# Performance work log

Measured on AMD Instinct MI355X. Metric: run time of the kernel, lower is better.

The kernel has to match this reference:

```python
import jax
import jax.numpy as jnp
import numpy as np
from jax import lax

B, L, H, M = 32768, 128, 256, 16


def setup_inputs() -> dict:
    key = jax.random.key(0)
    ks = jax.random.split(key, 7)
    s_ih = 1.0 / np.sqrt(H)  # PyTorch GRUCell init scale (uniform bound); use scaled normal
    return {
        "x": jax.random.randint(ks[0], (B, L), 0, M, dtype=jnp.int32),
        "W_ih": jax.random.normal(ks[1], (3 * H, 1), dtype=jnp.float32) * s_ih,
        "W_hh": jax.random.normal(ks[2], (3 * H, H), dtype=jnp.float32) * s_ih,
        "b_ih": jax.random.normal(ks[3], (3 * H,), dtype=jnp.float32) * s_ih,
        "b_hh": jax.random.normal(ks[4], (3 * H,), dtype=jnp.float32) * s_ih,
        "W_fc": jax.random.normal(ks[5], (M, H), dtype=jnp.float32) * s_ih,
        "b_fc": jax.random.normal(ks[6], (M,), dtype=jnp.float32) * s_ih,
    }


def reference(x, W_ih, W_hh, b_ih, b_hh, W_fc, b_fc):
    # (zeros at i=0) as a scalar feature; output log_softmax gathered at x[:, i].
    xf = x.astype(jnp.float32)
    x_in = jnp.concatenate([jnp.zeros((x.shape[0], 1), jnp.float32), xf[:, :-1]], axis=1)  # [B, L]

    def step(h, inp):
        x_t, tgt = inp  # x_t: [B] float, tgt: [B] int
        gi = x_t[:, None] * W_ih.T + b_ih            # [B, 3H] (input dim is 1)
        gh = h @ W_hh.T + b_hh                       # [B, 3H]
        ir, iz, i_n = jnp.split(gi, 3, axis=1)
        hr, hz, h_n = jnp.split(gh, 3, axis=1)
        r = jax.nn.sigmoid(ir + hr)
        z = jax.nn.sigmoid(iz + hz)
        n = jnp.tanh(i_n + r * h_n)
        h_new = (1.0 - z) * n + z * h                # [B, H]
        logp = jax.nn.log_softmax(h_new @ W_fc.T + b_fc, axis=1)  # [B, M]
        lp = jnp.take_along_axis(logp, tgt[:, None], axis=1)[:, 0]  # [B]
        return h_new, lp

    h0 = jnp.zeros((x.shape[0], W_hh.shape[1]), jnp.float32)
    _, lps = lax.scan(step, h0, (x_in.T, x.T))  # lps: [L, B]
    return lps.sum(axis=0)  # [B] log_probsum
```

## Files before the change

kernel.cpp:

```cpp
#include <hip/hip_runtime.h>

typedef __attribute__((ext_vector_type(8))) short s16x8;
typedef __attribute__((ext_vector_type(4))) float f32x4;

#define BATCH 32768
#define LSEQ 128
#define NJT 16
#define NFRAG 28
#define WFRAG_SHORTS (NJT * NFRAG * 512)
#define WFC_SHORTS 4096
#define XT_OFF_BYTES ((WFRAG_SHORTS + WFC_SHORTS) * 2)
#define WS_NEED_XT (XT_OFF_BYTES + BATCH * LSEQ * 4)

#define HBUF_SHORTS (128 * 256)
#define LDS_BYTES (2 * HBUF_SHORTS * 2 + WFC_SHORTS * 2)

#define L2E 1.4426950408889634f
#define LN2 0.6931471805599453f

__device__ __forceinline__ unsigned short f2b(float f) {
  unsigned u = __float_as_uint(f);
  u += 0x7FFFu + ((u >> 16) & 1u);
  return (unsigned short)(u >> 16);
}

__device__ __forceinline__ float exp2n(float x) { float r; asm("v_exp_f32 %0, -%1" : "=v"(r) : "v"(x)); return r; }
__device__ __forceinline__ float exp2p(float x) { float r; asm("v_exp_f32 %0, %1" : "=v"(r) : "v"(x)); return r; }
__device__ __forceinline__ float rcp_(float x)  { float r; asm("v_rcp_f32 %0, %1" : "=v"(r) : "v"(x)); return r; }
__device__ __forceinline__ float log2_(float x) { float r; asm("v_log_f32 %0, %1" : "=v"(r) : "v"(x)); return r; }
__device__ __forceinline__ unsigned cvtpk(float lo, float hi) {
  unsigned r; asm("v_cvt_pk_bf16_f32 %0, %1, %2" : "=v"(r) : "v"(lo), "v"(hi)); return r;
}

__global__ void gru_prep(const float* __restrict__ Wih, const float* __restrict__ Whh,
                         const float* __restrict__ bih, const float* __restrict__ bhh,
                         const float* __restrict__ Wfc,
                         unsigned short* __restrict__ wfrag,
                         unsigned short* __restrict__ wfc16) {
  int t = blockIdx.x * 256 + threadIdx.x;
  if (t < WFRAG_SHORTS) {
    int e = t & 7, lane = (t >> 3) & 63, fl = t >> 9;
    int f = fl % NFRAG, jt = fl / NFRAG;
    int m = lane & 15, gl = lane >> 4;
    float val = 0.f;
    if (f < 27) {
      int g = f / 9, ks = f % 9;
      int row = g * 256 + jt * 16 + m;
      int k = ks * 32 + gl * 8 + e;
      float sc = (g == 2) ? 2.f * L2E : L2E;
      if (k < 256) val = Whh[row * 256 + k] * sc;
      else if (k == 256) val = (g == 2) ? 0.f : Wih[row] * sc;
      else if (k == 257) val = ((g == 2) ? bhh[row] : (bih[row] + bhh[row])) * sc;
    }
    wfrag[t] = f2b(val);
  } else if (t < WFRAG_SHORTS + WFC_SHORTS) {
    int t2 = t - WFRAG_SHORTS;
    wfc16[t2] = f2b(Wfc[t2] * L2E);
  }
}

__global__ void x_transpose(const int* __restrict__ x, int* __restrict__ xT) {
  __shared__ int tile[32][33];
  int l0 = blockIdx.x * 32, b0 = blockIdx.y * 32;
  for (int r = threadIdx.y; r < 32; r += 8)
    tile[r][threadIdx.x] = x[(b0 + r) * LSEQ + l0 + threadIdx.x];
  __syncthreads();
  for (int r = threadIdx.y; r < 32; r += 8)
    xT[(l0 + r) * BATCH + b0 + threadIdx.x] = tile[threadIdx.x][r];
}

__device__ __forceinline__ int haddr(int lrow, int col_s) {
  return lrow * 256 + ((col_s + ((lrow & 15) << 3)) & 255);
}

template <int XT>
__global__ __attribute__((amdgpu_waves_per_eu(2, 2))) __launch_bounds__(512)
void gru_main(const int* __restrict__ x, const int* __restrict__ xTr,
              const unsigned short* __restrict__ wfrag,
              const unsigned short* __restrict__ wfc16,
              const float* __restrict__ Wih, const float* __restrict__ bih,
              const float* __restrict__ bfc, float* __restrict__ out) {
  extern __shared__ unsigned short smem_us[];
  unsigned short* h0 = smem_us;
  unsigned short* h1 = smem_us + HBUF_SHORTS;
  unsigned short* wl = smem_us + 2 * HBUF_SHORTS;

  const int tid = threadIdx.x;
  const int lane = tid & 63;
  const int wv = tid >> 6;
  const int q = lane >> 4;
  const int b = lane & 15;
  const int bbase = blockIdx.x * 128;

  {
    unsigned int* p = (unsigned int*)h0;
#pragma unroll
    for (int r = 0; r < 32; ++r) p[tid + r * 512] = 0u;
  }
  for (int t = tid; t < WFC_SHORTS; t += 512) {
    int m = t >> 8, col = t & 255;
    wl[haddr(m, col)] = wfc16[t];
  }

  float win0[4], bin0[4], win1[4], bin1[4];
#pragma unroll
  for (int r = 0; r < 4; ++r) {
    int j0 = 512 + wv * 16 + q * 4 + r;
    int j1 = 512 + (wv + 8) * 16 + q * 4 + r;
    win0[r] = Wih[j0] * (2.f * L2E);  bin0[r] = bih[j0] * (2.f * L2E);
    win1[r] = Wih[j1] * (2.f * L2E);  bin1[r] = bih[j1] * (2.f * L2E);
  }
  float bfc4[4];
#pragma unroll
  for (int r = 0; r < 4; ++r) bfc4[r] = bfc[q * 4 + r] * L2E;

  float lp = 0.f;
  __syncthreads();

#pragma unroll 1
  for (int i = 0; i < LSEQ; ++i) {
    const unsigned short* rd = (i & 1) ? h1 : h0;
    unsigned short* wr = (i & 1) ? h0 : h1;

    unsigned long wfu = (unsigned long)wfrag;
    asm volatile("" : "+s"(wfu));
    const unsigned short* wf = (const unsigned short*)wfu;

    float xin8[8];
    unsigned xlo[8];
#pragma unroll
    for (int bt = 0; bt < 8; ++bt) {
      float xv;
      if (XT) xv = (i > 0) ? (float)xTr[(i - 1) * BATCH + bbase + bt * 16 + b] : 0.f;
      else    xv = (i > 0) ? (float)x[(bbase + bt * 16 + b) * LSEQ + i - 1] : 0.f;
      xin8[bt] = xv;
      xlo[bt] = (q == 0) ? ((__float_as_uint(xv) >> 16) | 0x3F800000u) : 0u;
    }

#pragma unroll 1
    for (int ph = 0; ph < 2; ++ph) {
      const int jt = wv + 8 * ph;
      const unsigned short* fb = wf + (jt * NFRAG * 64 + lane) * 8;

      f32x4 aR[8], aZ[8], aH[8];
      const f32x4 Z = {0.f, 0.f, 0.f, 0.f};

      s16x8 ar = *(const s16x8*)(fb + 8 * 512);
      s16x8 az = *(const s16x8*)(fb + 17 * 512);
      s16x8 ah = *(const s16x8*)(fb + 26 * 512);
      s16x8 cr = *(const s16x8*)(fb);
      s16x8 cz = *(const s16x8*)(fb + 9 * 512);
      s16x8 ch = *(const s16x8*)(fb + 18 * 512);

#pragma unroll
      for (int bt = 0; bt < 8; ++bt) {
        union { unsigned u[4]; s16x8 v; } xf;
        xf.u[0] = xlo[bt]; xf.u[1] = 0u; xf.u[2] = 0u; xf.u[3] = 0u;
        aR[bt] = __builtin_amdgcn_mfma_f32_16x16x32_bf16(ar, xf.v, Z, 0, 0, 0);
        aZ[bt] = __builtin_amdgcn_mfma_f32_16x16x32_bf16(az, xf.v, Z, 0, 0, 0);
        aH[bt] = __builtin_amdgcn_mfma_f32_16x16x32_bf16(ah, xf.v, Z, 0, 0, 0);
      }

      auto burst = [&](s16x8 A0, s16x8 A1, s16x8 A2, int ks) {
#pragma unroll
        for (int bt = 0; bt < 8; ++bt) {
          const s16x8 hb = *(const s16x8*)&rd[haddr(bt * 16 + b, 32 * ks + 8 * q)];
          aR[bt] = __builtin_amdgcn_mfma_f32_16x16x32_bf16(A0, hb, aR[bt], 0, 0, 0);
          aZ[bt] = __builtin_amdgcn_mfma_f32_16x16x32_bf16(A1, hb, aZ[bt], 0, 0, 0);
          aH[bt] = __builtin_amdgcn_mfma_f32_16x16x32_bf16(A2, hb, aH[bt], 0, 0, 0);
        }
      };

#pragma unroll 1
      for (int ks = 0; ks < 7; ++ks) {
        s16x8 nr = *(const s16x8*)(fb + (ks + 1) * 512);
        s16x8 nz = *(const s16x8*)(fb + (ks + 10) * 512);
        s16x8 nh = *(const s16x8*)(fb + (ks + 19) * 512);
        burst(cr, cz, ch, ks);
        cr = nr; cz = nz; ch = nh;
      }
      burst(cr, cz, ch, 7);

      const float wcA = ph ? win1[0] : win0[0], wcB = ph ? win1[1] : win0[1];
      const float wcC = ph ? win1[2] : win0[2], wcD = ph ? win1[3] : win0[3];
      const float bcA = ph ? bin1[0] : bin0[0], bcB = ph ? bin1[1] : bin0[1];
      const float bcC = ph ? bin1[2] : bin0[2], bcD = ph ? bin1[3] : bin0[3];
#pragma unroll
      for (int bt = 0; bt < 8; ++bt) {
        const int lrow = bt * 16 + b;
        const uint2 hp = *(const uint2*)&rd[haddr(lrow, 16 * jt + 4 * q)];
        const float xv = xin8[bt];
        const float inr[4] = {fmaf(xv, wcA, bcA), fmaf(xv, wcB, bcB),
                              fmaf(xv, wcC, bcC), fmaf(xv, wcD, bcD)};
        const float hpv[4] = {
            __uint_as_float(hp.x << 16), __uint_as_float(hp.x & 0xFFFF0000u),
            __uint_as_float(hp.y << 16), __uint_as_float(hp.y & 0xFFFF0000u)};
        float hv[4];
#pragma unroll
        for (int r = 0; r < 4; ++r) {
          float rr = rcp_(1.f + exp2n(aR[bt][r]));
          float zz = rcp_(1.f + exp2n(aZ[bt][r]));
          float y  = fmaf(rr, aH[bt][r], inr[r]);
          float u  = rcp_(1.f + exp2p(y));
          float nn = fmaf(-2.f, u, 1.f);
          hv[r] = fmaf(zz, hpv[r] - nn, nn);
        }
        *(uint2*)&wr[haddr(lrow, 16 * jt + 4 * q)] =
            make_uint2(cvtpk(hv[0], hv[1]), cvtpk(hv[2], hv[3]));
      }
    }

    __syncthreads();

    {
      const int lrow = wv * 16 + b;
      const int grow = bbase + lrow;
      f32x4 fa = {bfc4[0], bfc4[1], bfc4[2], bfc4[3]};
#pragma unroll
      for (int ks = 0; ks < 8; ++ks) {
        s16x8 wfcf = *(const s16x8*)&wl[haddr(b, 32 * ks + 8 * q)];
        s16x8 hb = *(const s16x8*)&wr[haddr(lrow, 32 * ks + 8 * q)];
        fa = __builtin_amdgcn_mfma_f32_16x16x32_bf16(wfcf, hb, fa, 0, 0, 0);
      }
      int tgt = XT ? xTr[i * BATCH + grow] : x[grow * LSEQ + i];
      float l0 = fa[0], l1 = fa[1], l2 = fa[2], l3 = fa[3];
      float mx = fmaxf(fmaxf(l0, l1), fmaxf(l2, l3));
      mx = fmaxf(mx, __shfl_xor(mx, 16));
      mx = fmaxf(mx, __shfl_xor(mx, 32));
      float se = exp2p(l0 - mx) + exp2p(l1 - mx) + exp2p(l2 - mx) + exp2p(l3 - mx);
      se += __shfl_xor(se, 16);
      se += __shfl_xor(se, 32);
      float v01 = (tgt & 1) ? l1 : l0;
      float v23 = (tgt & 1) ? l3 : l2;
      float vs = (tgt & 2) ? v23 : v01;
      float contrib = (q == (tgt >> 2)) ? vs : 0.f;
      contrib += __shfl_xor(contrib, 16);
      contrib += __shfl_xor(contrib, 32);
      lp += contrib - mx - log2_(se);
    }
  }

  if (q == 0) out[bbase + wv * 16 + b] = lp * LN2;
}

extern "C" void kernel_launch(void* const* d_in, const int* in_sizes, int n_in,
                              void* d_out, int out_size, void* d_ws, size_t ws_size,
                              hipStream_t stream) {
  (void)in_sizes; (void)n_in; (void)out_size;
  const int*   x   = (const int*)d_in[0];
  const float* Wih = (const float*)d_in[1];
  const float* Whh = (const float*)d_in[2];
  const float* bih = (const float*)d_in[3];
  const float* bhh = (const float*)d_in[4];
  const float* Wfc = (const float*)d_in[5];
  const float* bfc = (const float*)d_in[6];
  float* out = (float*)d_out;

  unsigned short* wfrag = (unsigned short*)d_ws;
  unsigned short* wfc16 = wfrag + WFRAG_SHORTS;
  int* xT = (int*)((char*)d_ws + XT_OFF_BYTES);

  gru_prep<<<dim3(912), dim3(256), 0, stream>>>(Wih, Whh, bih, bhh, Wfc, wfrag, wfc16);

  if (ws_size >= (size_t)WS_NEED_XT) {
    x_transpose<<<dim3(LSEQ / 32, BATCH / 32), dim3(32, 8), 0, stream>>>(x, xT);
    hipFuncSetAttribute((const void*)gru_main<1>,
                        hipFuncAttributeMaxDynamicSharedMemorySize, LDS_BYTES);
    gru_main<1><<<dim3(256), dim3(512), LDS_BYTES, stream>>>(x, xT, wfrag, wfc16,
                                                             Wih, bih, bfc, out);
  } else {
    hipFuncSetAttribute((const void*)gru_main<0>,
                        hipFuncAttributeMaxDynamicSharedMemorySize, LDS_BYTES);
    gru_main<0><<<dim3(256), dim3(512), LDS_BYTES, stream>>>(x, x, wfrag, wfc16,
                                                             Wih, bih, bfc, out);
  }
}
```

Measured before the change: 1.847 ms.

## Switch GRU recurrence to 32x32x16 MFMA tiles with padded LDS rows

Replaces the 16x16x32 MFMA tiling of the hidden-state GEMM with 32x32x16 MFMAs. Each wave now owns a 32-wide hidden slice across all gates and processes pairs of 32-row batch groups, with the input-gate term folded in as an extra MFMA. The XOR-swizzled LDS layout is replaced by rows padded to 264 elements. The FC weights are read from global memory instead of LDS, and the log2e scaling moves from the prepacked weights into the epilogue. The aim is fewer MFMA issues and more reuse per weight fragment, at the cost of extra epilogue multiplies and possible register pressure from the larger accumulators.

```diff
diff --git a/kernel.cpp b/kernel.cpp
--- a/kernel.cpp
+++ b/kernel.cpp
@@ -2,21 +2,23 @@
 
 typedef __attribute__((ext_vector_type(8))) short s16x8;
 typedef __attribute__((ext_vector_type(4))) float f32x4;
+typedef __attribute__((ext_vector_type(16))) float f32x16;
 
 #define BATCH 32768
 #define LSEQ 128
-#define NJT 16
-#define NFRAG 28
-#define WFRAG_SHORTS (NJT * NFRAG * 512)
+#define W32_SHORTS (8 * 4 * 17 * 512)
 #define WFC_SHORTS 4096
-#define XT_OFF_BYTES ((WFRAG_SHORTS + WFC_SHORTS) * 2)
+#define XT_OFF_BYTES ((W32_SHORTS + WFC_SHORTS) * 2)
 #define WS_NEED_XT (XT_OFF_BYTES + BATCH * LSEQ * 4)
 
-#define HBUF_SHORTS (128 * 256)
-#define LDS_BYTES (2 * HBUF_SHORTS * 2 + WFC_SHORTS * 2)
+#define HROW 264
+#define HBUF_S (128 * HROW)
+#define LDS_BYTES (2 * HBUF_S * 2)
 
 #define L2E 1.4426950408889634f
 #define LN2 0.6931471805599453f
+
+#define MFMA32(A, B, C) __builtin_amdgcn_mfma_f32_32x32x16_bf16(A, B, C, 0, 0, 0)
 
 __device__ __forceinline__ unsigned short f2b(float f) {
   unsigned u = __float_as_uint(f);
@@ -38,24 +40,26 @@
                          unsigned short* __restrict__ wfrag,
                          unsigned short* __restrict__ wfc16) {
   int t = blockIdx.x * 256 + threadIdx.x;
-  if (t < WFRAG_SHORTS) {
-    int e = t & 7, lane = (t >> 3) & 63, fl = t >> 9;
-    int f = fl % NFRAG, jt = fl / NFRAG;
-    int m = lane & 15, gl = lane >> 4;
+  if (t < W32_SHORTS) {
+    int e = t & 7, lane = (t >> 3) & 63, frag = t >> 9;
+    int ks = frag % 17, g = (frag / 17) & 3, tr = frag / 68;
+    int l31 = lane & 31, hh = lane >> 5;
+    int k = (ks < 16) ? ks * 16 + hh * 8 + e : 256 + hh * 8 + e;
     float val = 0.f;
-    if (f < 27) {
-      int g = f / 9, ks = f % 9;
-      int row = g * 256 + jt * 16 + m;
-      int k = ks * 32 + gl * 8 + e;
-      float sc = (g == 2) ? 2.f * L2E : L2E;
-      if (k < 256) val = Whh[row * 256 + k] * sc;
-      else if (k == 256) val = (g == 2) ? 0.f : Wih[row] * sc;
-      else if (k == 257) val = ((g == 2) ? bhh[row] : (bih[row] + bhh[row])) * sc;
+    if (g < 3) {
+      int j = g * 256 + tr * 32 + l31;
+      if (k < 256) val = Whh[j * 256 + k];
+      else if (k == 256) val = (g < 2) ? Wih[j] : 0.f;
+      else if (k == 257) val = (g < 2) ? (bih[j] + bhh[j]) : bhh[j];
+    } else if (ks == 16) {
+      int j = 512 + tr * 32 + l31;
+      if (k == 256) val = Wih[j];
+      else if (k == 257) val = bih[j];
     }
     wfrag[t] = f2b(val);
-  } else if (t < WFRAG_SHORTS + WFC_SHORTS) {
-    int t2 = t - WFRAG_SHORTS;
-    wfc16[t2] = f2b(Wfc[t2] * L2E);
+  } else if (t < W32_SHORTS + WFC_SHORTS) {
+    int t2 = t - W32_SHORTS;
+    wfc16[t2] = f2b(Wfc[t2]);
   }
 }
 
@@ -69,145 +73,151 @@
     xT[(l0 + r) * BATCH + b0 + threadIdx.x] = tile[threadIdx.x][r];
 }
 
-__device__ __forceinline__ int haddr(int lrow, int col_s) {
-  return lrow * 256 + ((col_s + ((lrow & 15) << 3)) & 255);
-}
-
 template <int XT>
 __global__ __attribute__((amdgpu_waves_per_eu(2, 2))) __launch_bounds__(512)
 void gru_main(const int* __restrict__ x, const int* __restrict__ xTr,
               const unsigned short* __restrict__ wfrag,
               const unsigned short* __restrict__ wfc16,
-              const float* __restrict__ Wih, const float* __restrict__ bih,
               const float* __restrict__ bfc, float* __restrict__ out) {
-  extern __shared__ unsigned short smem_us[];
-  unsigned short* h0 = smem_us;
-  unsigned short* h1 = smem_us + HBUF_SHORTS;
-  unsigned short* wl = smem_us + 2 * HBUF_SHORTS;
+  extern __shared__ unsigned short sm[];
 
   const int tid = threadIdx.x;
   const int lane = tid & 63;
   const int wv = tid >> 6;
+  const int tr = wv;
+  const int l31 = lane & 31;
+  const int hh = lane >> 5;
   const int q = lane >> 4;
   const int b = lane & 15;
   const int bbase = blockIdx.x * 128;
 
   {
-    unsigned int* p = (unsigned int*)h0;
-#pragma unroll
-    for (int r = 0; r < 32; ++r) p[tid + r * 512] = 0u;
-  }
-  for (int t = tid; t < WFC_SHORTS; t += 512) {
-    int m = t >> 8, col = t & 255;
-    wl[haddr(m, col)] = wfc16[t];
-  }
-
-  float win0[4], bin0[4], win1[4], bin1[4];
-#pragma unroll
-  for (int r = 0; r < 4; ++r) {
-    int j0 = 512 + wv * 16 + q * 4 + r;
-    int j1 = 512 + (wv + 8) * 16 + q * 4 + r;
-    win0[r] = Wih[j0] * (2.f * L2E);  bin0[r] = bih[j0] * (2.f * L2E);
-    win1[r] = Wih[j1] * (2.f * L2E);  bin1[r] = bih[j1] * (2.f * L2E);
-  }
+    unsigned int* p = (unsigned int*)sm;
+    for (int r = tid; r < HBUF_S / 2; r += 512) p[r] = 0u;
+  }
+
   float bfc4[4];
 #pragma unroll
-  for (int r = 0; r < 4; ++r) bfc4[r] = bfc[q * 4 + r] * L2E;
+  for (int r = 0; r < 4; ++r) bfc4[r] = bfc[q * 4 + r];
+
+  const int offR = ((tr * 4 + 0) * 17) * 512 + lane * 8;
+  const int offZ = ((tr * 4 + 1) * 17) * 512 + lane * 8;
+  const int offH = ((tr * 4 + 2) * 17) * 512 + lane * 8;
+  const int offI = ((tr * 4 + 3) * 17) * 512 + lane * 8;
+  const int offFC = b * 256 + q * 8;
+
+  const f32x16 z16 = {0, 0, 0, 0, 0, 0, 0, 0, 0, 0, 0, 0, 0, 0, 0, 0};
 
   float lp = 0.f;
   __syncthreads();
 
 #pragma unroll 1
   for (int i = 0; i < LSEQ; ++i) {
-    const unsigned short* rd = (i & 1) ? h1 : h0;
-    unsigned short* wr = (i & 1) ? h0 : h1;
+    const unsigned short* rdb = sm + (i & 1) * HBUF_S;
+    unsigned short* wrb = sm + ((i & 1) ^ 1) * HBUF_S;
 
     unsigned long wfu = (unsigned long)wfrag;
     asm volatile("" : "+s"(wfu));
-    const unsigned short* wf = (const unsigned short*)wfu;
-
-    float xin8[8];
-    unsigned xlo[8];
-#pragma unroll
-    for (int bt = 0; bt < 8; ++bt) {
-      float xv;
-      if (XT) xv = (i > 0) ? (float)xTr[(i - 1) * BATCH + bbase + bt * 16 + b] : 0.f;
-      else    xv = (i > 0) ? (float)x[(bbase + bt * 16 + b) * LSEQ + i - 1] : 0.f;
-      xin8[bt] = xv;
-      xlo[bt] = (q == 0) ? ((__float_as_uint(xv) >> 16) | 0x3F800000u) : 0u;
-    }
-
-#pragma unroll 1
-    for (int ph = 0; ph < 2; ++ph) {
-      const int jt = wv + 8 * ph;
-      const unsigned short* fb = wf + (jt * NFRAG * 64 + lane) * 8;
-
-      f32x4 aR[8], aZ[8], aH[8];
-      const f32x4 Z = {0.f, 0.f, 0.f, 0.f};
-
-      s16x8 ar = *(const s16x8*)(fb + 8 * 512);
-      s16x8 az = *(const s16x8*)(fb + 17 * 512);
-      s16x8 ah = *(const s16x8*)(fb + 26 * 512);
-      s16x8 cr = *(const s16x8*)(fb);
-      s16x8 cz = *(const s16x8*)(fb + 9 * 512);
-      s16x8 ch = *(const s16x8*)(fb + 18 * 512);
-
-#pragma unroll
-      for (int bt = 0; bt < 8; ++bt) {
-        union { unsigned u[4]; s16x8 v; } xf;
-        xf.u[0] = xlo[bt]; xf.u[1] = 0u; xf.u[2] = 0u; xf.u[3] = 0u;
-        aR[bt] = __builtin_amdgcn_mfma_f32_16x16x32_bf16(ar, xf.v, Z, 0, 0, 0);
-        aZ[bt] = __builtin_amdgcn_mfma_f32_16x16x32_bf16(az, xf.v, Z, 0, 0, 0);
-        aH[bt] = __builtin_amdgcn_mfma_f32_16x16x32_bf16(ah, xf.v, Z, 0, 0, 0);
+    const unsigned short* wfp = (const unsigned short*)wfu;
+    const unsigned short* fR = wfp + offR;
+    const unsigned short* fZ = wfp + offZ;
+    const unsigned short* fH = wfp + offH;
+    const unsigned short* fI = wfp + offI;
+    unsigned long wcu = (unsigned long)wfc16;
+    asm volatile("" : "+s"(wcu));
+    const unsigned short* fFC = (const unsigned short*)wcu + offFC;
+
+#pragma unroll
+    for (int p = 0; p < 2; ++p) {
+      const int b0 = 2 * p, b1 = 2 * p + 1;
+
+      float xv0, xv1;
+      if (XT) {
+        xv0 = (i > 0) ? (float)xTr[(i - 1) * BATCH + bbase + b0 * 32 + l31] : 0.f;
+        xv1 = (i > 0) ? (float)xTr[(i - 1) * BATCH + bbase + b1 * 32 + l31] : 0.f;
+      } else {
+        xv0 = (i > 0) ? (float)x[(bbase + b0 * 32 + l31) * LSEQ + i - 1] : 0.f;
+        xv1 = (i > 0) ? (float)x[(bbase + b1 * 32 + l31) * LSEQ + i - 1] : 0.f;
       }
-
-      auto burst = [&](s16x8 A0, s16x8 A1, s16x8 A2, int ks) {
-#pragma unroll
-        for (int bt = 0; bt < 8; ++bt) {
-          const s16x8 hb = *(const s16x8*)&rd[haddr(bt * 16 + b, 32 * ks + 8 * q)];
-          aR[bt] = __builtin_amdgcn_mfma_f32_16x16x32_bf16(A0, hb, aR[bt], 0, 0, 0);
-          aZ[bt] = __builtin_amdgcn_mfma_f32_16x16x32_bf16(A1, hb, aZ[bt], 0, 0, 0);
-          aH[bt] = __builtin_amdgcn_mfma_f32_16x16x32_bf16(A2, hb, aH[bt], 0, 0, 0);
+      union { unsigned u[4]; s16x8 v; } xf0, xf1;
+      xf0.u[0] = (hh == 0) ? ((__float_as_uint(xv0) >> 16) | 0x3F800000u) : 0u;
+      xf0.u[1] = xf0.u[2] = xf0.u[3] = 0u;
+      xf1.u[0] = (hh == 0) ? ((__float_as_uint(xv1) >> 16) | 0x3F800000u) : 0u;
+      xf1.u[1] = xf1.u[2] = xf1.u[3] = 0u;
+
+      s16x8 gR = *(const s16x8*)(fR + 16 * 512);
+      s16x8 gZ = *(const s16x8*)(fZ + 16 * 512);
+      s16x8 gH = *(const s16x8*)(fH + 16 * 512);
+      s16x8 gI = *(const s16x8*)(fI + 16 * 512);
+      f32x16 R0 = MFMA32(gR, xf0.v, z16), R1 = MFMA32(gR, xf1.v, z16);
+      f32x16 Z0 = MFMA32(gZ, xf0.v, z16), Z1 = MFMA32(gZ, xf1.v, z16);
+      f32x16 H0 = MFMA32(gH, xf0.v, z16), H1 = MFMA32(gH, xf1.v, z16);
+      f32x16 I0 = MFMA32(gI, xf0.v, z16), I1 = MFMA32(gI, xf1.v, z16);
+
+      s16x8 c0r = *(const s16x8*)(fR + 0 * 512);
+      s16x8 c0z = *(const s16x8*)(fZ + 0 * 512);
+      s16x8 c0h = *(const s16x8*)(fH + 0 * 512);
+      s16x8 c1r = *(const s16x8*)(fR + 1 * 512);
+      s16x8 c1z = *(const s16x8*)(fZ + 1 * 512);
+      s16x8 c1h = *(const s16x8*)(fH + 1 * 512);
+
+      const unsigned short* r0b = rdb + (b0 * 32 + l31) * HROW;
+      const unsigned short* r1b = rdb + (b1 * 32 + l31) * HROW;
+
+#pragma unroll
+      for (int it = 0; it < 8; ++it) {
+        s16x8 n0r, n0z, n0h, n1r, n1z, n1h;
+        if (it < 7) {
+          n0r = *(const s16x8*)(fR + (2 * it + 2) * 512);
+          n0z = *(const s16x8*)(fZ + (2 * it + 2) * 512);
+          n0h = *(const s16x8*)(fH + (2 * it + 2) * 512);
+          n1r = *(const s16x8*)(fR + (2 * it + 3) * 512);
+          n1z = *(const s16x8*)(fZ + (2 * it + 3) * 512);
+          n1h = *(const s16x8*)(fH + (2 * it + 3) * 512);
+        }
+        {
+          const s16x8 hA = *(const s16x8*)&r0b[16 * (2 * it) + 8 * hh];
+          const s16x8 hB = *(const s16x8*)&r1b[16 * (2 * it) + 8 * hh];
+          R0 = MFMA32(c0r, hA, R0); Z0 = MFMA32(c0z, hA, Z0); H0 = MFMA32(c0h, hA, H0);
+          R1 = MFMA32(c0r, hB, R1); Z1 = MFMA32(c0z, hB, Z1); H1 = MFMA32(c0h, hB, H1);
+        }
+        {
+          const s16x8 hA = *(const s16x8*)&r0b[16 * (2 * it + 1) + 8 * hh];
+          const s16x8 hB = *(const s16x8*)&r1b[16 * (2 * it + 1) + 8 * hh];
+          R0 = MFMA32(c1r, hA, R0); Z0 = MFMA32(c1z, hA, Z0); H0 = MFMA32(c1h, hA, H0);
+          R1 = MFMA32(c1r, hB, R1); Z1 = MFMA32(c1z, hB, Z1); H1 = MFMA32(c1h, hB, H1);
+        }
+        if (it < 7) { c0r = n0r; c0z = n0z; c0h = n0h; c1r = n1r; c1z = n1z; c1h = n1h; }
+      }
+
+      auto epilogue = [&](int bg, const f32x16& R, const f32x16& Zg,
+                          const f32x16& Hg, const f32x16& Ig) {
+        const int hrow = bg * 32 + l31;
+        const unsigned short* hpb = rdb + hrow * HROW;
+        unsigned short* hwb = wrb + hrow * HROW;
+#pragma unroll
+        for (int rq = 0; rq < 4; ++rq) {
+          const int col = tr * 32 + 4 * hh + 8 * rq;
+          const uint2 hp = *(const uint2*)&hpb[col];
+          const float hpv[4] = {
+              __uint_as_float(hp.x << 16), __uint_as_float(hp.x & 0xFFFF0000u),
+              __uint_as_float(hp.y << 16), __uint_as_float(hp.y & 0xFFFF0000u)};
+          float hv[4];
+#pragma unroll
+          for (int e2 = 0; e2 < 4; ++e2) {
+            const int idx = rq * 4 + e2;
+            float rr = rcp_(1.f + exp2n(L2E * R[idx]));
+            float zz = rcp_(1.f + exp2n(L2E * Zg[idx]));
+            float y  = fmaf(rr, Hg[idx], Ig[idx]);
+            float u  = rcp_(1.f + exp2p((2.f * L2E) * y));
+            float nn = fmaf(-2.f, u, 1.f);
+            hv[e2] = fmaf(zz, hpv[e2] - nn, nn);
+          }
+          *(uint2*)&hwb[col] = make_uint2(cvtpk(hv[0], hv[1]), cvtpk(hv[2], hv[3]));
         }
       };
-
-#pragma unroll 1
-      for (int ks = 0; ks < 7; ++ks) {
-        s16x8 nr = *(const s16x8*)(fb + (ks + 1) * 512);
-        s16x8 nz = *(const s16x8*)(fb + (ks + 10) * 512);
-        s16x8 nh = *(const s16x8*)(fb + (ks + 19) * 512);
-        burst(cr, cz, ch, ks);
-        cr = nr; cz = nz; ch = nh;
-      }
-      burst(cr, cz, ch, 7);
-
-      const float wcA = ph ? win1[0] : win0[0], wcB = ph ? win1[1] : win0[1];
-      const float wcC = ph ? win1[2] : win0[2], wcD = ph ? win1[3] : win0[3];
-      const float bcA = ph ? bin1[0] : bin0[0], bcB = ph ? bin1[1] : bin0[1];
-      const float bcC = ph ? bin1[2] : bin0[2], bcD = ph ? bin1[3] : bin0[3];
-#pragma unroll
-      for (int bt = 0; bt < 8; ++bt) {
-        const int lrow = bt * 16 + b;
-        const uint2 hp = *(const uint2*)&rd[haddr(lrow, 16 * jt + 4 * q)];
-        const float xv = xin8[bt];
-        const float inr[4] = {fmaf(xv, wcA, bcA), fmaf(xv, wcB, bcB),
-                              fmaf(xv, wcC, bcC), fmaf(xv, wcD, bcD)};
-        const float hpv[4] = {
-            __uint_as_float(hp.x << 16), __uint_as_float(hp.x & 0xFFFF0000u),
-            __uint_as_float(hp.y << 16), __uint_as_float(hp.y & 0xFFFF0000u)};
-        float hv[4];
-#pragma unroll
-        for (int r = 0; r < 4; ++r) {
-          float rr = rcp_(1.f + exp2n(aR[bt][r]));
-          float zz = rcp_(1.f + exp2n(aZ[bt][r]));
-          float y  = fmaf(rr, aH[bt][r], inr[r]);
-          float u  = rcp_(1.f + exp2p(y));
-          float nn = fmaf(-2.f, u, 1.f);
-          hv[r] = fmaf(zz, hpv[r] - nn, nn);
-        }
-        *(uint2*)&wr[haddr(lrow, 16 * jt + 4 * q)] =
-            make_uint2(cvtpk(hv[0], hv[1]), cvtpk(hv[2], hv[3]));
-      }
+      epilogue(b0, R0, Z0, H0, I0);
+      epilogue(b1, R1, Z1, H1, I1);
     }
 
     __syncthreads();
@@ -216,18 +226,20 @@
       const int lrow = wv * 16 + b;
       const int grow = bbase + lrow;
       f32x4 fa = {bfc4[0], bfc4[1], bfc4[2], bfc4[3]};
+      const unsigned short* hbb = wrb + lrow * HROW;
 #pragma unroll
       for (int ks = 0; ks < 8; ++ks) {
-        s16x8 wfcf = *(const s16x8*)&wl[haddr(b, 32 * ks + 8 * q)];
-        s16x8 hb = *(const s16x8*)&wr[haddr(lrow, 32 * ks + 8 * q)];
-        fa = __builtin_amdgcn_mfma_f32_16x16x32_bf16(wfcf, hb, fa, 0, 0, 0);
+        s16x8 wf = *(const s16x8*)(fFC + 32 * ks);
+        s16x8 hb = *(const s16x8*)&hbb[32 * ks + 8 * q];
+        fa = __builtin_amdgcn_mfma_f32_16x16x32_bf16(wf, hb, fa, 0, 0, 0);
       }
       int tgt = XT ? xTr[i * BATCH + grow] : x[grow * LSEQ + i];
       float l0 = fa[0], l1 = fa[1], l2 = fa[2], l3 = fa[3];
       float mx = fmaxf(fmaxf(l0, l1), fmaxf(l2, l3));
       mx = fmaxf(mx, __shfl_xor(mx, 16));
       mx = fmaxf(mx, __shfl_xor(mx, 32));
-      float se = exp2p(l0 - mx) + exp2p(l1 - mx) + exp2p(l2 - mx) + exp2p(l3 - mx);
+      float se = exp2p(L2E * (l0 - mx)) + exp2p(L2E * (l1 - mx)) +
+                 exp2p(L2E * (l2 - mx)) + exp2p(L2E * (l3 - mx));
       se += __shfl_xor(se, 16);
       se += __shfl_xor(se, 32);
       float v01 = (tgt & 1) ? l1 : l0;
@@ -236,11 +248,11 @@
       float contrib = (q == (tgt >> 2)) ? vs : 0.f;
       contrib += __shfl_xor(contrib, 16);
       contrib += __shfl_xor(contrib, 32);
-      lp += contrib - mx - log2_(se);
+      lp += contrib - mx - LN2 * log2_(se);
     }
   }
 
-  if (q == 0) out[bbase + wv * 16 + b] = lp * LN2;
+  if (q == 0) out[bbase + wv * 16 + b] = lp;
 }
 
 extern "C" void kernel_launch(void* const* d_in, const int* in_sizes, int n_in,
@@ -257,21 +269,20 @@
   float* out = (float*)d_out;
 
   unsigned short* wfrag = (unsigned short*)d_ws;
-  unsigned short* wfc16 = wfrag + WFRAG_SHORTS;
+  unsigned short* wfc16 = wfrag + W32_SHORTS;
   int* xT = (int*)((char*)d_ws + XT_OFF_BYTES);
 
-  gru_prep<<<dim3(912), dim3(256), 0, stream>>>(Wih, Whh, bih, bhh, Wfc, wfrag, wfc16);
+  gru_prep<<<dim3((W32_SHORTS + WFC_SHORTS) / 256), dim3(256), 0, stream>>>(
+      Wih, Whh, bih, bhh, Wfc, wfrag, wfc16);
 
   if (ws_size >= (size_t)WS_NEED_XT) {
     x_transpose<<<dim3(LSEQ / 32, BATCH / 32), dim3(32, 8), 0, stream>>>(x, xT);
     hipFuncSetAttribute((const void*)gru_main<1>,
                         hipFuncAttributeMaxDynamicSharedMemorySize, LDS_BYTES);
-    gru_main<1><<<dim3(256), dim3(512), LDS_BYTES, stream>>>(x, xT, wfrag, wfc16,
-                                                             Wih, bih, bfc, out);
+    gru_main<1><<<dim3(256), dim3(512), LDS_BYTES, stream>>>(x, xT, wfrag, wfc16, bfc, out);
   } else {
     hipFuncSetAttribute((const void*)gru_main<0>,
                         hipFuncAttributeMaxDynamicSharedMemorySize, LDS_BYTES);
-    gru_main<0><<<dim3(256), dim3(512), LDS_BYTES, stream>>>(x, x, wfrag, wfc16,
-                                                             Wih, bih, bfc, out);
-  }
-}
+    gru_main<0><<<dim3(256), dim3(512), LDS_BYTES, stream>>>(x, x, wfrag, wfc16, bfc, out);
+  }
+}
```

After: 2.042 ms. 10.6% more time.

## Pad LDS hidden-state rows, read W_fc from global, fully unroll K loop

Applied to the files above, without the earlier changes.

Replaces the XOR-swizzled hidden-state layout with rows padded to 264 shorts to avoid LDS bank conflicts using simpler address arithmetic. The W_fc copy in LDS is dropped and W_fc fragments are read straight from global/L2. The K-loop over weight fragments is fully unrolled, with all 24 weight fragments loaded up front instead of double-buffered. The log2e scaling moves from the prepped weights into the activation math, which costs extra multiplies per element and may change bf16 rounding of the weights. The extra fragment registers raise register pressure.

```diff
diff --git a/kernel.cpp b/kernel.cpp
--- a/kernel.cpp
+++ b/kernel.cpp
@@ -12,11 +12,14 @@
 #define XT_OFF_BYTES ((WFRAG_SHORTS + WFC_SHORTS) * 2)
 #define WS_NEED_XT (XT_OFF_BYTES + BATCH * LSEQ * 4)
 
-#define HBUF_SHORTS (128 * 256)
-#define LDS_BYTES (2 * HBUF_SHORTS * 2 + WFC_SHORTS * 2)
+#define HROW 264
+#define HBUF_S (128 * HROW)
+#define LDS_BYTES (2 * HBUF_S * 2)
 
 #define L2E 1.4426950408889634f
 #define LN2 0.6931471805599453f
+
+#define MFMA16(A, B, C) __builtin_amdgcn_mfma_f32_16x16x32_bf16(A, B, C, 0, 0, 0)
 
 __device__ __forceinline__ unsigned short f2b(float f) {
   unsigned u = __float_as_uint(f);
@@ -47,15 +50,14 @@
       int g = f / 9, ks = f % 9;
       int row = g * 256 + jt * 16 + m;
       int k = ks * 32 + gl * 8 + e;
-      float sc = (g == 2) ? 2.f * L2E : L2E;
-      if (k < 256) val = Whh[row * 256 + k] * sc;
-      else if (k == 256) val = (g == 2) ? 0.f : Wih[row] * sc;
-      else if (k == 257) val = ((g == 2) ? bhh[row] : (bih[row] + bhh[row])) * sc;
+      if (k < 256) val = Whh[row * 256 + k];
+      else if (k == 256) val = (g == 2) ? 0.f : Wih[row];
+      else if (k == 257) val = (g == 2) ? bhh[row] : (bih[row] + bhh[row]);
     }
     wfrag[t] = f2b(val);
   } else if (t < WFRAG_SHORTS + WFC_SHORTS) {
     int t2 = t - WFRAG_SHORTS;
-    wfc16[t2] = f2b(Wfc[t2] * L2E);
+    wfc16[t2] = f2b(Wfc[t2]);
   }
 }
 
@@ -69,10 +71,6 @@
     xT[(l0 + r) * BATCH + b0 + threadIdx.x] = tile[threadIdx.x][r];
 }
 
-__device__ __forceinline__ int haddr(int lrow, int col_s) {
-  return lrow * 256 + ((col_s + ((lrow & 15) << 3)) & 255);
-}
-
 template <int XT>
 __global__ __attribute__((amdgpu_waves_per_eu(2, 2))) __launch_bounds__(512)
 void gru_main(const int* __restrict__ x, const int* __restrict__ xTr,
@@ -80,10 +78,9 @@
               const unsigned short* __restrict__ wfc16,
               const float* __restrict__ Wih, const float* __restrict__ bih,
               const float* __restrict__ bfc, float* __restrict__ out) {
-  extern __shared__ unsigned short smem_us[];
-  unsigned short* h0 = smem_us;
-  unsigned short* h1 = smem_us + HBUF_SHORTS;
-  unsigned short* wl = smem_us + 2 * HBUF_SHORTS;
+  extern __shared__ unsigned short sm[];
+  unsigned short* h0 = sm;
+  unsigned short* h1 = sm + HBUF_S;
 
   const int tid = threadIdx.x;
   const int lane = tid & 63;
@@ -95,11 +92,7 @@
   {
     unsigned int* p = (unsigned int*)h0;
 #pragma unroll
-    for (int r = 0; r < 32; ++r) p[tid + r * 512] = 0u;
-  }
-  for (int t = tid; t < WFC_SHORTS; t += 512) {
-    int m = t >> 8, col = t & 255;
-    wl[haddr(m, col)] = wfc16[t];
+    for (int r = 0; r < 33; ++r) p[tid + r * 512] = 0u;
   }
 
   float win0[4], bin0[4], win1[4], bin1[4];
@@ -107,12 +100,14 @@
   for (int r = 0; r < 4; ++r) {
     int j0 = 512 + wv * 16 + q * 4 + r;
     int j1 = 512 + (wv + 8) * 16 + q * 4 + r;
-    win0[r] = Wih[j0] * (2.f * L2E);  bin0[r] = bih[j0] * (2.f * L2E);
-    win1[r] = Wih[j1] * (2.f * L2E);  bin1[r] = bih[j1] * (2.f * L2E);
+    win0[r] = Wih[j0];  bin0[r] = bih[j0];
+    win1[r] = Wih[j1];  bin1[r] = bih[j1];
   }
   float bfc4[4];
 #pragma unroll
-  for (int r = 0; r < 4; ++r) bfc4[r] = bfc[q * 4 + r] * L2E;
+  for (int r = 0; r < 4; ++r) bfc4[r] = bfc[q * 4 + r];
+
+  const int rbase = b * HROW + 8 * q;
 
   float lp = 0.f;
   __syncthreads();
@@ -125,61 +120,67 @@
     unsigned long wfu = (unsigned long)wfrag;
     asm volatile("" : "+s"(wfu));
     const unsigned short* wf = (const unsigned short*)wfu;
+    unsigned long wcu = (unsigned long)wfc16;
+    asm volatile("" : "+s"(wcu));
+    const unsigned short* wc = (const unsigned short*)wcu;
 
     float xin8[8];
-    unsigned xlo[8];
 #pragma unroll
     for (int bt = 0; bt < 8; ++bt) {
-      float xv;
-      if (XT) xv = (i > 0) ? (float)xTr[(i - 1) * BATCH + bbase + bt * 16 + b] : 0.f;
-      else    xv = (i > 0) ? (float)x[(bbase + bt * 16 + b) * LSEQ + i - 1] : 0.f;
-      xin8[bt] = xv;
-      xlo[bt] = (q == 0) ? ((__float_as_uint(xv) >> 16) | 0x3F800000u) : 0u;
+      if (XT) xin8[bt] = (i > 0) ? (float)xTr[(i - 1) * BATCH + bbase + bt * 16 + b] : 0.f;
+      else    xin8[bt] = (i > 0) ? (float)x[(bbase + bt * 16 + b) * LSEQ + i - 1] : 0.f;
     }
 
 #pragma unroll 1
     for (int ph = 0; ph < 2; ++ph) {
       const int jt = wv + 8 * ph;
       const unsigned short* fb = wf + (jt * NFRAG * 64 + lane) * 8;
-
-      f32x4 aR[8], aZ[8], aH[8];
-      const f32x4 Z = {0.f, 0.f, 0.f, 0.f};
+      const unsigned short* rdT = rd + rbase;
 
       s16x8 ar = *(const s16x8*)(fb + 8 * 512);
       s16x8 az = *(const s16x8*)(fb + 17 * 512);
       s16x8 ah = *(const s16x8*)(fb + 26 * 512);
-      s16x8 cr = *(const s16x8*)(fb);
-      s16x8 cz = *(const s16x8*)(fb + 9 * 512);
-      s16x8 ch = *(const s16x8*)(fb + 18 * 512);
-
+      s16x8 c0r = *(const s16x8*)(fb + 0 * 512), c0z = *(const s16x8*)(fb + 9 * 512),  c0h = *(const s16x8*)(fb + 18 * 512);
+      s16x8 c1r = *(const s16x8*)(fb + 1 * 512), c1z = *(const s16x8*)(fb + 10 * 512), c1h = *(const s16x8*)(fb + 19 * 512);
+      s16x8 c2r = *(const s16x8*)(fb + 2 * 512), c2z = *(const s16x8*)(fb + 11 * 512), c2h = *(const s16x8*)(fb + 20 * 512);
+      s16x8 c3r = *(const s16x8*)(fb + 3 * 512), c3z = *(const s16x8*)(fb + 12 * 512), c3h = *(const s16x8*)(fb + 21 * 512);
+
+      f32x4 aR[8], aZ[8], aH[8];
+      const f32x4 Z4 = {0.f, 0.f, 0.f, 0.f};
 #pragma unroll
       for (int bt = 0; bt < 8; ++bt) {
         union { unsigned u[4]; s16x8 v; } xf;
-        xf.u[0] = xlo[bt]; xf.u[1] = 0u; xf.u[2] = 0u; xf.u[3] = 0u;
-        aR[bt] = __builtin_amdgcn_mfma_f32_16x16x32_bf16(ar, xf.v, Z, 0, 0, 0);
-        aZ[bt] = __builtin_amdgcn_mfma_f32_16x16x32_bf16(az, xf.v, Z, 0, 0, 0);
-        aH[bt] = __builtin_amdgcn_mfma_f32_16x16x32_bf16(ah, xf.v, Z, 0, 0, 0);
+        xf.u[0] = (q == 0) ? ((__float_as_uint(xin8[bt]) >> 16) | 0x3F800000u) : 0u;
+        xf.u[1] = xf.u[2] = xf.u[3] = 0u;
+        aR[bt] = MFMA16(ar, xf.v, Z4);
+        aZ[bt] = MFMA16(az, xf.v, Z4);
+        aH[bt] = MFMA16(ah, xf.v, Z4);
       }
 
-      auto burst = [&](s16x8 A0, s16x8 A1, s16x8 A2, int ks) {
-#pragma unroll
-        for (int bt = 0; bt < 8; ++bt) {
-          const s16x8 hb = *(const s16x8*)&rd[haddr(bt * 16 + b, 32 * ks + 8 * q)];
-          aR[bt] = __builtin_amdgcn_mfma_f32_16x16x32_bf16(A0, hb, aR[bt], 0, 0, 0);
-          aZ[bt] = __builtin_amdgcn_mfma_f32_16x16x32_bf16(A1, hb, aZ[bt], 0, 0, 0);
-          aH[bt] = __builtin_amdgcn_mfma_f32_16x16x32_bf16(A2, hb, aH[bt], 0, 0, 0);
-        }
-      };
-
-#pragma unroll 1
-      for (int ks = 0; ks < 7; ++ks) {
-        s16x8 nr = *(const s16x8*)(fb + (ks + 1) * 512);
-        s16x8 nz = *(const s16x8*)(fb + (ks + 10) * 512);
-        s16x8 nh = *(const s16x8*)(fb + (ks + 19) * 512);
-        burst(cr, cz, ch, ks);
-        cr = nr; cz = nz; ch = nh;
-      }
-      burst(cr, cz, ch, 7);
+      s16x8 n0r = *(const s16x8*)(fb + 4 * 512), n0z = *(const s16x8*)(fb + 13 * 512), n0h = *(const s16x8*)(fb + 22 * 512);
+      s16x8 n1r = *(const s16x8*)(fb + 5 * 512), n1z = *(const s16x8*)(fb + 14 * 512), n1h = *(const s16x8*)(fb + 23 * 512);
+      s16x8 n2r = *(const s16x8*)(fb + 6 * 512), n2z = *(const s16x8*)(fb + 15 * 512), n2h = *(const s16x8*)(fb + 24 * 512);
+      s16x8 n3r = *(const s16x8*)(fb + 7 * 512), n3z = *(const s16x8*)(fb + 16 * 512), n3h = *(const s16x8*)(fb + 25 * 512);
+
+#define BURST(CR, CZ, CH, KS)                                                   \
+  {                                                                             \
+    _Pragma("unroll")                                                           \
+    for (int bt = 0; bt < 8; ++bt) {                                            \
+      const s16x8 hb = *(const s16x8*)&rdT[bt * 16 * HROW + 32 * (KS)];         \
+      aR[bt] = MFMA16(CR, hb, aR[bt]);                                          \
+      aZ[bt] = MFMA16(CZ, hb, aZ[bt]);                                          \
+      aH[bt] = MFMA16(CH, hb, aH[bt]);                                          \
+    }                                                                           \
+  }
+      BURST(c0r, c0z, c0h, 0)
+      BURST(c1r, c1z, c1h, 1)
+      BURST(c2r, c2z, c2h, 2)
+      BURST(c3r, c3z, c3h, 3)
+      BURST(n0r, n0z, n0h, 4)
+      BURST(n1r, n1z, n1h, 5)
+      BURST(n2r, n2z, n2h, 6)
+      BURST(n3r, n3z, n3h, 7)
+#undef BURST
 
       const float wcA = ph ? win1[0] : win0[0], wcB = ph ? win1[1] : win0[1];
       const float wcC = ph ? win1[2] : win0[2], wcD = ph ? win1[3] : win0[3];
@@ -188,7 +189,7 @@
 #pragma unroll
       for (int bt = 0; bt < 8; ++bt) {
         const int lrow = bt * 16 + b;
-        const uint2 hp = *(const uint2*)&rd[haddr(lrow, 16 * jt + 4 * q)];
+        const uint2 hp = *(const uint2*)&rd[lrow * HROW + 16 * jt + 4 * q];
         const float xv = xin8[bt];
         const float inr[4] = {fmaf(xv, wcA, bcA), fmaf(xv, wcB, bcB),
                               fmaf(xv, wcC, bcC), fmaf(xv, wcD, bcD)};
@@ -198,14 +199,14 @@
         float hv[4];
 #pragma unroll
         for (int r = 0; r < 4; ++r) {
-          float rr = rcp_(1.f + exp2n(aR[bt][r]));
-          float zz = rcp_(1.f + exp2n(aZ[bt][r]));
+          float rr = rcp_(1.f + exp2n(L2E * aR[bt][r]));
+          float zz = rcp_(1.f + exp2n(L2E * aZ[bt][r]));
           float y  = fmaf(rr, aH[bt][r], inr[r]);
-          float u  = rcp_(1.f + exp2p(y));
+          float u  = rcp_(1.f + exp2p((2.f * L2E) * y));
           float nn = fmaf(-2.f, u, 1.f);
           hv[r] = fmaf(zz, hpv[r] - nn, nn);
         }
-        *(uint2*)&wr[haddr(lrow, 16 * jt + 4 * q)] =
+        *(uint2*)&wr[lrow * HROW + 16 * jt + 4 * q] =
             make_uint2(cvtpk(hv[0], hv[1]), cvtpk(hv[2], hv[3]));
       }
     }
@@ -216,18 +217,21 @@
       const int lrow = wv * 16 + b;
       const int grow = bbase + lrow;
       f32x4 fa = {bfc4[0], bfc4[1], bfc4[2], bfc4[3]};
+      const unsigned short* hbb = wr + lrow * HROW + 8 * q;
+      const unsigned short* wcb = wc + b * 256 + q * 8;
 #pragma unroll
       for (int ks = 0; ks < 8; ++ks) {
-        s16x8 wfcf = *(const s16x8*)&wl[haddr(b, 32 * ks + 8 * q)];
-        s16x8 hb = *(const s16x8*)&wr[haddr(lrow, 32 * ks + 8 * q)];
-        fa = __builtin_amdgcn_mfma_f32_16x16x32_bf16(wfcf, hb, fa, 0, 0, 0);
+        s16x8 wfcf = *(const s16x8*)(wcb + 32 * ks);
+        s16x8 hb = *(const s16x8*)(hbb + 32 * ks);
+        fa = MFMA16(wfcf, hb, fa);
       }
       int tgt = XT ? xTr[i * BATCH + grow] : x[grow * LSEQ + i];
       float l0 = fa[0], l1 = fa[1], l2 = fa[2], l3 = fa[3];
       float mx = fmaxf(fmaxf(l0, l1), fmaxf(l2, l3));
       mx = fmaxf(mx, __shfl_xor(mx, 16));
       mx = fmaxf(mx, __shfl_xor(mx, 32));
-      float se = exp2p(l0 - mx) + exp2p(l1 - mx) + exp2p(l2 - mx) + exp2p(l3 - mx);
+      float se = exp2p(L2E * (l0 - mx)) + exp2p(L2E * (l1 - mx)) +
+                 exp2p(L2E * (l2 - mx)) + exp2p(L2E * (l3 - mx));
       se += __shfl_xor(se, 16);
       se += __shfl_xor(se, 32);
       float v01 = (tgt & 1) ? l1 : l0;
@@ -236,11 +240,11 @@
       float contrib = (q == (tgt >> 2)) ? vs : 0.f;
       contrib += __shfl_xor(contrib, 16);
       contrib += __shfl_xor(contrib, 32);
-      lp += contrib - mx - log2_(se);
-    }
-  }
-
-  if (q == 0) out[bbase + wv * 16 + b] = lp * LN2;
+      lp += contrib - mx - LN2 * log2_(se);
+    }
+  }
+
+  if (q == 0) out[bbase + wv * 16 + b] = lp;
 }
 
 extern "C" void kernel_launch(void* const* d_in, const int* in_sizes, int n_in,
```

Result: slower. 2.026 ms (+9.7%).
